# Kernel tuning notes

Hardware: AMD Instinct MI355X
Metric: run time of the kernel (lower is better)

Reference implementation:

```python
import jax, jax.numpy as jnp
import numpy as np

B, T, D, UNITS = 32, 2048, 1024, 1024


def setup_inputs() -> dict:
    key = jax.random.key(0)
    ks = jax.random.split(key, 9)
    values = jax.random.normal(ks[0], (B, T, D), dtype=jnp.float32)
    query = jax.random.normal(ks[1], (B, D), dtype=jnp.float32)
    # mask: 1.0 where position is masked out, 0.0 otherwise
    mask = jax.random.randint(ks[2], (B, T), 0, 2).astype(jnp.float32)
    # Dense params (keras Dense: y = x @ W + b)
    W1 = jax.random.normal(ks[3], (D, UNITS), dtype=jnp.float32) / np.sqrt(D)
    b1 = jnp.zeros((UNITS,), dtype=jnp.float32)
    W2 = jax.random.normal(ks[4], (D, UNITS), dtype=jnp.float32) / np.sqrt(D)
    b2 = jnp.zeros((UNITS,), dtype=jnp.float32)
    V = jax.random.normal(ks[5], (UNITS, 1), dtype=jnp.float32) / np.sqrt(UNITS)
    bV = jnp.zeros((1,), dtype=jnp.float32)
    return {"values": values, "query": query, "mask": mask,
            "W1": W1, "b1": b1, "W2": W2, "b2": b2, "V": V, "bV": bV}


def reference(values, query, mask, W1, b1, W2, b2, V, bV):
    # values: [B,T,D], query: [B,D], mask: [B,T] (1.0 = masked)
    proj_v = jnp.einsum('btd,du->btu', values, W1) + b1          # [B,T,U]
    proj_q = (query @ W2 + b2)[:, None, :]                        # [B,1,U]
    score = jnp.tanh(proj_v + proj_q) @ V + bV                    # [B,T,1]
    score = score + mask[:, :, None] * (-1e9)                     # mask out
    attention_weights = jax.nn.softmax(score, axis=1)             # [B,T,1]
    context_vector = jnp.sum(attention_weights * values, axis=1)  # [B,D]
    return (context_vector, attention_weights)
```

## Files before the change

### kernel.cpp

```cpp
#include <hip/hip_runtime.h>
#include <hip/hip_bf16.h>


typedef __bf16 bf16x8 __attribute__((ext_vector_type(8)));
typedef __bf16 bf16x4 __attribute__((ext_vector_type(4)));
typedef float  f32x4  __attribute__((ext_vector_type(4)));

#define B_  32
#define T_  2048
#define D_  1024
#define U_  1024
#define BT_ (B_*T_)

#define WS_W1T    ((size_t)0)
#define WS_PROJQ  ((size_t)(2u*1024*1024))
#define WS_SCORE  ((size_t)(2u*1024*1024 + 128u*1024))
#define WS_VALB   ((size_t)(4u*1024*1024))
#define WS_NEEDED (WS_VALB + (size_t)BT_ * D_ * 2)

__device__ __forceinline__ float tanh_fast(float x) {
    const float e = __expf(2.0f * x);
    return 1.0f - __fdividef(2.0f, e + 1.0f);
}

__device__ __forceinline__ void glls16(const void* g, void* l) {
    __builtin_amdgcn_global_load_lds(
        (const __attribute__((address_space(1))) void*)g,
        (__attribute__((address_space(3))) void*)l, 16, 0, 0);
}

__global__ void init_kernel(const float* __restrict__ b1, const float* __restrict__ b2,
                            float* __restrict__ projq, float* __restrict__ score) {
    int i = blockIdx.x * 256 + threadIdx.x;
    if (i < B_ * U_) {
        projq[i] = b1[i & (U_ - 1)] + b2[i & (U_ - 1)];
    } else {
        score[i - B_ * U_] = 0.0f;
    }
}

__global__ void convert_kernel(const float* __restrict__ v, __bf16* __restrict__ o) {
    const size_t i = ((size_t)blockIdx.x * 256 + threadIdx.x) * 8;
    const float4 a = *(const float4*)(v + i);
    const float4 b = *(const float4*)(v + i + 4);
    bf16x8 h;
    h[0] = (__bf16)a.x; h[1] = (__bf16)a.y; h[2] = (__bf16)a.z; h[3] = (__bf16)a.w;
    h[4] = (__bf16)b.x; h[5] = (__bf16)b.y; h[6] = (__bf16)b.z; h[7] = (__bf16)b.w;
    *(bf16x8*)(o + i) = h;
}

__global__ void w1_transpose_kernel(const float* __restrict__ W1, __bf16* __restrict__ W1T) {
    __shared__ float tile[64][65];
    const int bx = blockIdx.x & 15;
    const int by = blockIdx.x >> 4;
    const int tid = threadIdx.x;
    const int j  = tid & 63;
    const int i0 = tid >> 6;
#pragma unroll
    for (int p = 0; p < 16; ++p) {
        const int i = i0 + p * 4;
        tile[i][j] = W1[(size_t)(by * 64 + i) * U_ + bx * 64 + j];
    }
    __syncthreads();
#pragma unroll
    for (int p = 0; p < 16; ++p) {
        const int i = i0 + p * 4;
        W1T[(size_t)(bx * 64 + i) * D_ + by * 64 + j] = (__bf16)tile[j][i];
    }
}

__global__ void projq_kernel(const float* __restrict__ query, const float* __restrict__ W2,
                             float* __restrict__ projq) {
    __shared__ float q[128];
    const int b  = blockIdx.x >> 3;
    const int dc = blockIdx.x & 7;
    const int tid = threadIdx.x;
    if (tid < 128) q[tid] = query[(size_t)b * D_ + dc * 128 + tid];
    __syncthreads();
    const int u0 = tid * 4;
    float a0 = 0.f, a1 = 0.f, a2 = 0.f, a3 = 0.f;
    for (int d = 0; d < 128; ++d) {
        const float4 w = *(const float4*)(W2 + (size_t)(dc * 128 + d) * U_ + u0);
        const float qd = q[d];
        a0 = fmaf(qd, w.x, a0); a1 = fmaf(qd, w.y, a1);
        a2 = fmaf(qd, w.z, a2); a3 = fmaf(qd, w.w, a3);
    }
    float* p = projq + (size_t)b * U_ + u0;
    atomicAdd(p + 0, a0); atomicAdd(p + 1, a1);
    atomicAdd(p + 2, a2); atomicAdd(p + 3, a3);
}

__global__ __launch_bounds__(256, 4)
void score_kernel_bf16(const __bf16* __restrict__ valb, const __bf16* __restrict__ W1T,
                       const float* __restrict__ projq, const float* __restrict__ V,
                       float* __restrict__ score) {
    __shared__ __attribute__((aligned(16))) __bf16 Al[128 * 32];
    __shared__ __attribute__((aligned(16))) __bf16 Bl[128 * 32];

    const int tid = threadIdx.x;
    const int xcd  = blockIdx.x & 7;
    const int slot = blockIdx.x >> 3;
    const int rowblk = xcd * 64 + (slot >> 3);
    const int utile  = slot & 7;
    const int wave = tid >> 6, lane = tid & 63;
    const int quad = lane >> 4, l15 = lane & 15;
    const int wr = (wave >> 1) * 64;
    const int wc = (wave & 1) * 64;

    const __bf16* Ab = valb + ((size_t)rowblk * 128 + (tid >> 2)) * D_ + (tid & 3) * 8;
    const __bf16* Bb = W1T + ((size_t)utile * 128 + (tid >> 2)) * D_ + (tid & 3) * 8;
    __bf16* Ald = Al + wave * 512;
    __bf16* Bld = Bl + wave * 512;

    f32x4 acc[4][4];
#pragma unroll
    for (int i = 0; i < 4; ++i)
#pragma unroll
        for (int j = 0; j < 4; ++j) {
            f32x4 z = {0.f, 0.f, 0.f, 0.f};
            acc[i][j] = z;
        }

    for (int kk = 0; kk < D_; kk += 32) {
        glls16(Ab + kk,            Ald);
        glls16(Ab + 64 * D_ + kk,  Ald + 2048);
        glls16(Bb + kk,            Bld);
        glls16(Bb + 64 * D_ + kk,  Bld + 2048);
        __syncthreads();

        bf16x8 af[4];
#pragma unroll
        for (int mt = 0; mt < 4; ++mt)
            af[mt] = *(const bf16x8*)(Al + (wr + mt * 16 + l15) * 32 + quad * 8);
#pragma unroll
        for (int nt = 0; nt < 4; ++nt) {
            const bf16x8 bfr = *(const bf16x8*)(Bl + (wc + nt * 16 + l15) * 32 + quad * 8);
#pragma unroll
            for (int mt = 0; mt < 4; ++mt)
                acc[mt][nt] = __builtin_amdgcn_mfma_f32_16x16x32_bf16(af[mt], bfr, acc[mt][nt], 0, 0, 0);
        }
        __syncthreads();
    }

    const int b = rowblk >> 4;
    const float* pq = projq + (size_t)b * U_ + utile * 128 + wc;
    const float* Vp = V + utile * 128 + wc;
    const size_t rowbase = (size_t)rowblk * 128 + wr;
#pragma unroll
    for (int mt = 0; mt < 4; ++mt) {
        float s0 = 0.f, s1 = 0.f, s2 = 0.f, s3 = 0.f;
#pragma unroll
        for (int nt = 0; nt < 4; ++nt) {
            const int u = nt * 16 + l15;
            const float pqu = pq[u];
            const float vu  = Vp[u];
            s0 += tanh_fast(acc[mt][nt][0] + pqu) * vu;
            s1 += tanh_fast(acc[mt][nt][1] + pqu) * vu;
            s2 += tanh_fast(acc[mt][nt][2] + pqu) * vu;
            s3 += tanh_fast(acc[mt][nt][3] + pqu) * vu;
        }
        float s[4] = {s0, s1, s2, s3};
#pragma unroll
        for (int r = 0; r < 4; ++r) {
            float v = s[r];
            v += __shfl_xor(v, 1);
            v += __shfl_xor(v, 2);
            v += __shfl_xor(v, 4);
            v += __shfl_xor(v, 8);
            if (l15 == 0)
                atomicAdd(&score[rowbase + mt * 16 + quad * 4 + r], v);
        }
    }
}

__global__ __launch_bounds__(512, 2)
void score_kernel_f32(const float* __restrict__ values, const __bf16* __restrict__ W1T,
                      const float* __restrict__ projq, const float* __restrict__ V,
                      float* __restrict__ score) {
    __shared__ __attribute__((aligned(16))) __bf16 Al[64][40];
    __shared__ __attribute__((aligned(16))) __bf16 Bl[512][40];
    const int tid    = threadIdx.x;
    const int rowblk = blockIdx.x >> 1;
    const int nhalf  = blockIdx.x & 1;
    const int wave = tid >> 6, lane = tid & 63;
    const int quad = lane >> 4, l15 = lane & 15;
    const float*  Abase = values + (size_t)rowblk * 64 * D_;
    const __bf16* Bbase = W1T + (size_t)nhalf * 512 * D_;
    const int ar = tid >> 3, ac = (tid & 7) * 4;
    const int br = tid >> 2, bc = (tid & 3) * 8;
    f32x4 acc[4][4];
#pragma unroll
    for (int i = 0; i < 4; ++i)
#pragma unroll
        for (int j = 0; j < 4; ++j) { f32x4 z = {0.f,0.f,0.f,0.f}; acc[i][j] = z; }
    for (int kk = 0; kk < D_; kk += 32) {
        {
            const float4 v = *(const float4*)(Abase + (size_t)ar * D_ + kk + ac);
            bf16x4 h;
            h[0] = (__bf16)v.x; h[1] = (__bf16)v.y; h[2] = (__bf16)v.z; h[3] = (__bf16)v.w;
            *(bf16x4*)(&Al[ar][ac]) = h;
        }
#pragma unroll
        for (int p = 0; p < 4; ++p) {
            const int rr = p * 128 + br;
            const bf16x8 w = *(const bf16x8*)(Bbase + (size_t)rr * D_ + kk + bc);
            *(bf16x8*)(&Bl[rr][bc]) = w;
        }
        __syncthreads();
        bf16x8 af[4];
#pragma unroll
        for (int mt = 0; mt < 4; ++mt)
            af[mt] = *(const bf16x8*)(&Al[mt * 16 + l15][quad * 8]);
#pragma unroll
        for (int nt = 0; nt < 4; ++nt) {
            const bf16x8 bfr = *(const bf16x8*)(&Bl[wave * 64 + nt * 16 + l15][quad * 8]);
#pragma unroll
            for (int mt = 0; mt < 4; ++mt)
                acc[mt][nt] = __builtin_amdgcn_mfma_f32_16x16x32_bf16(af[mt], bfr, acc[mt][nt], 0, 0, 0);
        }
        __syncthreads();
    }
    const int b = rowblk >> 5;
    const size_t rowbase = (size_t)rowblk * 64;
    const float* pq = projq + (size_t)b * U_;
    const int ub = nhalf * 512 + wave * 64;
#pragma unroll
    for (int mt = 0; mt < 4; ++mt) {
        float s0 = 0.f, s1 = 0.f, s2 = 0.f, s3 = 0.f;
#pragma unroll
        for (int nt = 0; nt < 4; ++nt) {
            const int u = ub + nt * 16 + l15;
            const float pqu = pq[u];
            const float vu  = V[u];
            s0 += tanh_fast(acc[mt][nt][0] + pqu) * vu;
            s1 += tanh_fast(acc[mt][nt][1] + pqu) * vu;
            s2 += tanh_fast(acc[mt][nt][2] + pqu) * vu;
            s3 += tanh_fast(acc[mt][nt][3] + pqu) * vu;
        }
        float s[4] = {s0, s1, s2, s3};
#pragma unroll
        for (int r = 0; r < 4; ++r) {
            float v = s[r];
            v += __shfl_xor(v, 1);
            v += __shfl_xor(v, 2);
            v += __shfl_xor(v, 4);
            v += __shfl_xor(v, 8);
            if (l15 == 0)
                atomicAdd(&score[rowbase + mt * 16 + quad * 4 + r], v);
        }
    }
}

__global__ void softmax_kernel(const float* __restrict__ score, const float* __restrict__ mask,
                               const float* __restrict__ bV, float* __restrict__ out) {
    const int b = blockIdx.x;
    const int tid = threadIdx.x;
    const float bv = bV[0];
    float s[8];
    float lmax = -3.0e38f;
#pragma unroll
    for (int i = 0; i < 8; ++i) {
        const int t = tid + i * 256;
        const float v = score[(size_t)b * T_ + t] + bv + mask[(size_t)b * T_ + t] * (-1.0e9f);
        s[i] = v;
        lmax = fmaxf(lmax, v);
    }
#pragma unroll
    for (int m = 1; m < 64; m <<= 1) lmax = fmaxf(lmax, __shfl_xor(lmax, m));
    __shared__ float redm[4], reds[4];
    if ((tid & 63) == 0) redm[tid >> 6] = lmax;
    __syncthreads();
    const float M = fmaxf(fmaxf(redm[0], redm[1]), fmaxf(redm[2], redm[3]));
    float lsum = 0.f;
#pragma unroll
    for (int i = 0; i < 8; ++i) { s[i] = __expf(s[i] - M); lsum += s[i]; }
#pragma unroll
    for (int m = 1; m < 64; m <<= 1) lsum += __shfl_xor(lsum, m);
    if ((tid & 63) == 0) reds[tid >> 6] = lsum;
    __syncthreads();
    const float inv = 1.0f / (reds[0] + reds[1] + reds[2] + reds[3]);
#pragma unroll
    for (int i = 0; i < 8; ++i)
        out[(size_t)B_ * D_ + (size_t)b * T_ + tid + i * 256] = s[i] * inv;
}

__global__ void context_kernel(const float* __restrict__ values, const float* __restrict__ attn,
                               float* __restrict__ out) {
    const int b  = blockIdx.x >> 4;
    const int dc = blockIdx.x & 15;
    const int tid = threadIdx.x;
    __shared__ float a[T_];
#pragma unroll
    for (int i = 0; i < 8; ++i) a[tid + i * 256] = attn[(size_t)b * T_ + tid + i * 256];
    __syncthreads();
    const int dl = (tid & 15) * 4;
    const int tg = tid >> 4;
    const float* vb = values + (size_t)b * T_ * D_ + dc * 64 + dl;
    f32x4 acc = {0.f, 0.f, 0.f, 0.f};
#pragma unroll 4
    for (int t = tg; t < T_; t += 16) {
        const float4 v = *(const float4*)(vb + (size_t)t * D_);
        const float w = a[t];
        acc[0] = fmaf(w, v.x, acc[0]);
        acc[1] = fmaf(w, v.y, acc[1]);
        acc[2] = fmaf(w, v.z, acc[2]);
        acc[3] = fmaf(w, v.w, acc[3]);
    }
    __shared__ __attribute__((aligned(16))) float red[16][64];
    *(f32x4*)(&red[tg][dl]) = acc;
    __syncthreads();
    if (tid < 64) {
        float s = 0.f;
#pragma unroll
        for (int g = 0; g < 16; ++g) s += red[g][tid];
        out[(size_t)b * D_ + dc * 64 + tid] = s;
    }
}

extern "C" void kernel_launch(void* const* d_in, const int* in_sizes, int n_in,
                              void* d_out, int out_size, void* d_ws, size_t ws_size,
                              hipStream_t stream) {
    const float* values = (const float*)d_in[0];
    const float* query  = (const float*)d_in[1];
    const float* mask   = (const float*)d_in[2];
    const float* W1     = (const float*)d_in[3];
    const float* b1     = (const float*)d_in[4];
    const float* W2     = (const float*)d_in[5];
    const float* b2     = (const float*)d_in[6];
    const float* V      = (const float*)d_in[7];
    const float* bV     = (const float*)d_in[8];
    float* out = (float*)d_out;

    char* ws = (char*)d_ws;
    __bf16* W1T   = (__bf16*)(ws + WS_W1T);
    float*  projq = (float*)(ws + WS_PROJQ);
    float*  score = (float*)(ws + WS_SCORE);
    __bf16* valb  = (__bf16*)(ws + WS_VALB);

    init_kernel<<<dim3(384), dim3(256), 0, stream>>>(b1, b2, projq, score);
    w1_transpose_kernel<<<dim3(256), dim3(256), 0, stream>>>(W1, W1T);
    projq_kernel<<<dim3(256), dim3(256), 0, stream>>>(query, W2, projq);
    if (ws_size >= WS_NEEDED) {
        convert_kernel<<<dim3(32768), dim3(256), 0, stream>>>(values, valb);
        score_kernel_bf16<<<dim3(4096), dim3(256), 0, stream>>>(valb, W1T, projq, V, score);
    } else {
        score_kernel_f32<<<dim3(2048), dim3(512), 0, stream>>>(values, W1T, projq, V, score);
    }
    softmax_kernel<<<dim3(32), dim3(256), 0, stream>>>(score, mask, bV, out);
    context_kernel<<<dim3(512), dim3(256), 0, stream>>>(values, out + B_ * D_, out);
}
```

Measured before the change: 637.3 us.

## Replace bf16 score GEMM with 256x256 double-buffered phased MFMA kernel

Rewrites the bf16 score GEMM to use 256x256 tiles per 512-thread block, with BK=64. It adds double-buffered LDS with async global-to-LDS loads issued ahead of compute, an XOR-swizzled LDS layout, and raw ds_read_b128. MFMA work is split into four phases with barriers and setprio so loads overlap the math. This targets LDS/global bandwidth and load latency in the previous 128x128 single-buffered loop. The cost is higher register and LDS pressure, plus fragile hand-tuned waitcnt sequencing.

```diff
diff --git a/kernel.cpp b/kernel.cpp
--- a/kernel.cpp
+++ b/kernel.cpp
@@ -4,6 +4,7 @@
 
 typedef __bf16 bf16x8 __attribute__((ext_vector_type(8)));
 typedef __bf16 bf16x4 __attribute__((ext_vector_type(4)));
+typedef short  s16x8  __attribute__((ext_vector_type(8)));
 typedef float  f32x4  __attribute__((ext_vector_type(4)));
 
 #define B_  32
@@ -90,74 +91,143 @@
     atomicAdd(p + 2, a2); atomicAdd(p + 3, a3);
 }
 
-__global__ __launch_bounds__(256, 4)
-void score_kernel_bf16(const __bf16* __restrict__ valb, const __bf16* __restrict__ W1T,
-                       const float* __restrict__ projq, const float* __restrict__ V,
-                       float* __restrict__ score) {
-    __shared__ __attribute__((aligned(16))) __bf16 Al[128 * 32];
-    __shared__ __attribute__((aligned(16))) __bf16 Bl[128 * 32];
-
-    const int tid = threadIdx.x;
-    const int xcd  = blockIdx.x & 7;
-    const int slot = blockIdx.x >> 3;
-    const int rowblk = xcd * 64 + (slot >> 3);
-    const int utile  = slot & 7;
-    const int wave = tid >> 6, lane = tid & 63;
-    const int quad = lane >> 4, l15 = lane & 15;
-    const int wr = (wave >> 1) * 64;
-    const int wc = (wave & 1) * 64;
-
-    const __bf16* Ab = valb + ((size_t)rowblk * 128 + (tid >> 2)) * D_ + (tid & 3) * 8;
-    const __bf16* Bb = W1T + ((size_t)utile * 128 + (tid >> 2)) * D_ + (tid & 3) * 8;
-    __bf16* Ald = Al + wave * 512;
-    __bf16* Bld = Bl + wave * 512;
-
-    f32x4 acc[4][4];
-#pragma unroll
-    for (int i = 0; i < 4; ++i)
-#pragma unroll
-        for (int j = 0; j < 4; ++j) {
-            f32x4 z = {0.f, 0.f, 0.f, 0.f};
-            acc[i][j] = z;
-        }
-
-    for (int kk = 0; kk < D_; kk += 32) {
-        glls16(Ab + kk,            Ald);
-        glls16(Ab + 64 * D_ + kk,  Ald + 2048);
-        glls16(Bb + kk,            Bld);
-        glls16(Bb + 64 * D_ + kk,  Bld + 2048);
-        __syncthreads();
-
-        bf16x8 af[4];
-#pragma unroll
-        for (int mt = 0; mt < 4; ++mt)
-            af[mt] = *(const bf16x8*)(Al + (wr + mt * 16 + l15) * 32 + quad * 8);
+
+#define SC_LDSB 32768
+
+__global__ __launch_bounds__(512, 2)
+void score_kernel_8ph(const __bf16* __restrict__ valb, const __bf16* __restrict__ W1T,
+                      const float* __restrict__ projq, const float* __restrict__ V,
+                      float* __restrict__ score) {
+    __shared__ __attribute__((aligned(16))) __bf16 lds[2 * SC_LDSB];
+
+    const int tid  = threadIdx.x;
+    const int bid  = blockIdx.x;
+    const int xcd  = bid & 7;
+    const int sl   = bid >> 3;
+    const int mblk = xcd * 32 + (sl >> 2);
+    const int nblk = sl & 3;
+
+    const int wv   = tid >> 6;
+    const int lane = tid & 63;
+    const int wm   = wv >> 2;
+    const int wn   = wv & 3;
+    const int l15  = lane & 15, quad = lane >> 4;
+    const int e    = l15 & 7;
+    const int sl0  = ((quad)     ^ e) * 8;
+    const int sl1  = ((quad + 4) ^ e) * 8;
+    const int offA0 = wm * 8192 + l15 * 64 + sl0;
+    const int offA1 = wm * 8192 + l15 * 64 + sl1;
+    const int offB0 = 16384 + (wn >> 1) * 8192 + ((wn & 1) * 64 + l15) * 64 + sl0;
+    const int offB1 = 16384 + (wn >> 1) * 8192 + ((wn & 1) * 64 + l15) * 64 + sl1;
+
+    const int srow = lane >> 3;
+    const int scol = ((lane & 7) ^ srow) * 8;
+    const __bf16* aS = valb + ((size_t)mblk * 256 + wv * 8 + srow) * D_ + scol;
+    const __bf16* bS = W1T  + ((size_t)nblk * 256 + wv * 8 + srow) * D_ + scol;
+    __bf16* aD = lds + wv * 512;
+    __bf16* bD = lds + 16384 + wv * 512;
+
+#define DSR(dst, off) do { s16x8 _t;                                            \
+    asm volatile("ds_read_b128 %0, %1" : "=v"(_t)                              \
+        : "v"((const __attribute__((address_space(3))) __bf16*)(lds + (off)))); \
+    (dst) = __builtin_bit_cast(bf16x8, _t); } while (0)
+
+#define STA(CB, H, KT) do {                                                     \
+    glls16(aS + (size_t)((H)*128     ) * D_ + (KT)*64, aD + (CB) + (H)*8192);        \
+    glls16(aS + (size_t)((H)*128 + 64) * D_ + (KT)*64, aD + (CB) + (H)*8192 + 4096); \
+    } while (0)
+#define STB(CB, H, KT) do {                                                     \
+    glls16(bS + (size_t)((H)*128     ) * D_ + (KT)*64, bD + (CB) + (H)*8192);        \
+    glls16(bS + (size_t)((H)*128 + 64) * D_ + (KT)*64, bD + (CB) + (H)*8192 + 4096); \
+    } while (0)
+
+#define PH_SYNC do { __builtin_amdgcn_s_barrier();                              \
+    asm volatile("s_waitcnt lgkmcnt(0)" ::: "memory");                          \
+    __builtin_amdgcn_sched_barrier(0);                                          \
+    __builtin_amdgcn_s_setprio(1); } while (0)
+#define PH_END do { __builtin_amdgcn_s_setprio(0);                              \
+    __builtin_amdgcn_s_barrier(); } while (0)
+
+#define MQ(ML, NL) do {                                                         \
+    _Pragma("unroll") for (int mi = 0; mi < 4; ++mi)                            \
+    _Pragma("unroll") for (int ni = 0; ni < 2; ++ni) {                          \
+        acc[(ML)+mi][(NL)+ni] = __builtin_amdgcn_mfma_f32_16x16x32_bf16(        \
+            afr[mi][0], bfr[(NL)+ni][0], acc[(ML)+mi][(NL)+ni], 0, 0, 0);       \
+        acc[(ML)+mi][(NL)+ni] = __builtin_amdgcn_mfma_f32_16x16x32_bf16(        \
+            afr[mi][1], bfr[(NL)+ni][1], acc[(ML)+mi][(NL)+ni], 0, 0, 0);       \
+    } } while (0)
+
+#define TILE(KT, CB, DOA, DOB, VM) do {                                         \
+                                 \
+    _Pragma("unroll") for (int m = 0; m < 4; ++m) {                             \
+        DSR(afr[m][0], (CB) + offA0 + m*1024);                                  \
+        DSR(afr[m][1], (CB) + offA1 + m*1024); }                                \
+    _Pragma("unroll") for (int n = 0; n < 2; ++n) {                             \
+        DSR(bfr[n][0], (CB) + offB0 + n*1024);                                  \
+        DSR(bfr[n][1], (CB) + offB1 + n*1024); }                                \
+    if (DOA) STA((CB) ^ SC_LDSB, 0, (KT)+1);                                    \
+    PH_SYNC; MQ(0, 0); PH_END;                                                  \
+                                          \
+    _Pragma("unroll") for (int n = 0; n < 2; ++n) {                             \
+        DSR(bfr[2+n][0], (CB) + offB0 + (2+n)*1024);                            \
+        DSR(bfr[2+n][1], (CB) + offB1 + (2+n)*1024); }                          \
+    if (DOA) STA((CB) ^ SC_LDSB, 1, (KT)+1);                                    \
+    PH_SYNC; MQ(0, 2); PH_END;                                                  \
+                                          \
+    _Pragma("unroll") for (int m = 0; m < 4; ++m) {                             \
+        DSR(afr[m][0], (CB) + offA0 + (4+m)*1024);                              \
+        DSR(afr[m][1], (CB) + offA1 + (4+m)*1024); }                            \
+    if (DOB) STB((CB), 0, (KT)+2);                                              \
+    PH_SYNC; MQ(4, 0); PH_END;                                                  \
+             \
+    if (DOB) STB((CB), 1, (KT)+2);                                              \
+    __builtin_amdgcn_s_barrier();                                               \
+    __builtin_amdgcn_sched_barrier(0);                                          \
+    __builtin_amdgcn_s_setprio(1);                                              \
+    MQ(4, 2);                                                                   \
+    __builtin_amdgcn_s_setprio(0);                                              \
+    if ((VM) == 4)      asm volatile("s_waitcnt vmcnt(4)" ::: "memory");        \
+    else if ((VM) == 0) asm volatile("s_waitcnt vmcnt(0)" ::: "memory");        \
+    __builtin_amdgcn_s_barrier();                                               \
+} while (0)
+
+    bf16x8 afr[4][2];
+    bf16x8 bfr[4][2];
+    f32x4  acc[8][4];
+#pragma unroll
+    for (int i = 0; i < 8; ++i)
+#pragma unroll
+        for (int j = 0; j < 4; ++j) { f32x4 z = {0.f, 0.f, 0.f, 0.f}; acc[i][j] = z; }
+
+    STA(0, 0, 0); STA(0, 1, 0); STB(0, 0, 0); STB(0, 1, 0);
+    STB(SC_LDSB, 0, 1); STB(SC_LDSB, 1, 1);
+    asm volatile("s_waitcnt vmcnt(4)" ::: "memory");
+    __builtin_amdgcn_s_barrier();
+
+#pragma unroll 1
+    for (int tt = 0; tt < 14; tt += 2) {
+        TILE(tt,     0,       1, 1, 4);
+        TILE(tt + 1, SC_LDSB, 1, 1, 4);
+    }
+    TILE(14, 0,       1, 0, 0);
+    TILE(15, SC_LDSB, 0, 0, -1);
+
+    const int bq = mblk >> 3;
+    const float* pq = projq + (size_t)bq * U_ + nblk * 256 + wn * 64;
+    const float* Vp = V + nblk * 256 + wn * 64;
+    float pqu[4], vu[4];
+#pragma unroll
+    for (int nt = 0; nt < 4; ++nt) { pqu[nt] = pq[nt * 16 + l15]; vu[nt] = Vp[nt * 16 + l15]; }
+    const size_t rowbase = (size_t)mblk * 256 + (size_t)wm * 128;
+#pragma unroll
+    for (int mt = 0; mt < 8; ++mt) {
+        float s0 = 0.f, s1 = 0.f, s2 = 0.f, s3 = 0.f;
 #pragma unroll
         for (int nt = 0; nt < 4; ++nt) {
-            const bf16x8 bfr = *(const bf16x8*)(Bl + (wc + nt * 16 + l15) * 32 + quad * 8);
-#pragma unroll
-            for (int mt = 0; mt < 4; ++mt)
-                acc[mt][nt] = __builtin_amdgcn_mfma_f32_16x16x32_bf16(af[mt], bfr, acc[mt][nt], 0, 0, 0);
-        }
-        __syncthreads();
-    }
-
-    const int b = rowblk >> 4;
-    const float* pq = projq + (size_t)b * U_ + utile * 128 + wc;
-    const float* Vp = V + utile * 128 + wc;
-    const size_t rowbase = (size_t)rowblk * 128 + wr;
-#pragma unroll
-    for (int mt = 0; mt < 4; ++mt) {
-        float s0 = 0.f, s1 = 0.f, s2 = 0.f, s3 = 0.f;
-#pragma unroll
-        for (int nt = 0; nt < 4; ++nt) {
-            const int u = nt * 16 + l15;
-            const float pqu = pq[u];
-            const float vu  = Vp[u];
-            s0 += tanh_fast(acc[mt][nt][0] + pqu) * vu;
-            s1 += tanh_fast(acc[mt][nt][1] + pqu) * vu;
-            s2 += tanh_fast(acc[mt][nt][2] + pqu) * vu;
-            s3 += tanh_fast(acc[mt][nt][3] + pqu) * vu;
+            s0 += tanh_fast(acc[mt][nt][0] + pqu[nt]) * vu[nt];
+            s1 += tanh_fast(acc[mt][nt][1] + pqu[nt]) * vu[nt];
+            s2 += tanh_fast(acc[mt][nt][2] + pqu[nt]) * vu[nt];
+            s3 += tanh_fast(acc[mt][nt][3] + pqu[nt]) * vu[nt];
         }
         float s[4] = {s0, s1, s2, s3};
 #pragma unroll
@@ -171,6 +241,13 @@
                 atomicAdd(&score[rowbase + mt * 16 + quad * 4 + r], v);
         }
     }
+#undef DSR
+#undef STA
+#undef STB
+#undef PH_SYNC
+#undef PH_END
+#undef MQ
+#undef TILE
 }
 
 __global__ __launch_bounds__(512, 2)
@@ -342,7 +419,7 @@
     projq_kernel<<<dim3(256), dim3(256), 0, stream>>>(query, W2, projq);
     if (ws_size >= WS_NEEDED) {
         convert_kernel<<<dim3(32768), dim3(256), 0, stream>>>(values, valb);
-        score_kernel_bf16<<<dim3(4096), dim3(256), 0, stream>>>(valb, W1T, projq, V, score);
+        score_kernel_8ph<<<dim3(1024), dim3(512), 0, stream>>>(valb, W1T, projq, V, score);
     } else {
         score_kernel_f32<<<dim3(2048), dim3(512), 0, stream>>>(values, W1T, projq, V, score);
     }
```

Result: faster. 615.4 us (-3.4%).

## Double-buffer score GEMM with 128x256 tiles, swizzled LDS, and bf16 context read

Applied to the files above, without the earlier changes.

Replaces the bf16 score GEMM with a 512-thread kernel that computes 128x256 output tiles and double-buffers the LDS stages so the next K-slice is loaded while the current one runs on MFMA. A single barrier per step replaces two, and an XOR swizzle on LDS slots is meant to cut bank conflicts. The context reduction now reads the bf16 copy of values instead of fp32, which halves that kernel's memory traffic but adds bf16 rounding error to the context output. The larger LDS footprint and register use may lower occupancy.

```diff
diff --git a/kernel.cpp b/kernel.cpp
--- a/kernel.cpp
+++ b/kernel.cpp
@@ -90,74 +90,96 @@
     atomicAdd(p + 2, a2); atomicAdd(p + 3, a3);
 }
 
-__global__ __launch_bounds__(256, 4)
-void score_kernel_bf16(const __bf16* __restrict__ valb, const __bf16* __restrict__ W1T,
-                       const float* __restrict__ projq, const float* __restrict__ V,
-                       float* __restrict__ score) {
-    __shared__ __attribute__((aligned(16))) __bf16 Al[128 * 32];
-    __shared__ __attribute__((aligned(16))) __bf16 Bl[128 * 32];
-
-    const int tid = threadIdx.x;
-    const int xcd  = blockIdx.x & 7;
-    const int slot = blockIdx.x >> 3;
-    const int rowblk = xcd * 64 + (slot >> 3);
-    const int utile  = slot & 7;
-    const int wave = tid >> 6, lane = tid & 63;
-    const int quad = lane >> 4, l15 = lane & 15;
-    const int wr = (wave >> 1) * 64;
-    const int wc = (wave & 1) * 64;
-
-    const __bf16* Ab = valb + ((size_t)rowblk * 128 + (tid >> 2)) * D_ + (tid & 3) * 8;
-    const __bf16* Bb = W1T + ((size_t)utile * 128 + (tid >> 2)) * D_ + (tid & 3) * 8;
-    __bf16* Ald = Al + wave * 512;
-    __bf16* Bld = Bl + wave * 512;
+
+#define SC_A_ELE 4096
+#define SC_B_ELE 8192
+#define SC_BUF   (SC_A_ELE + SC_B_ELE)
+
+__global__ __launch_bounds__(512, 4)
+void score_kernel_occ(const __bf16* __restrict__ valb, const __bf16* __restrict__ W1T,
+                      const float* __restrict__ projq, const float* __restrict__ V,
+                      float* __restrict__ score) {
+    __shared__ __attribute__((aligned(16))) __bf16 lds[2 * SC_BUF];
+
+    const int tid  = threadIdx.x;
+    const int bid  = blockIdx.x;
+    const int xcd  = bid & 7;
+    const int sl   = bid >> 3;
+    const int mblk = xcd * 64 + (sl >> 2);
+    const int nblk = sl & 3;
+
+    const int wv   = tid >> 6;
+    const int lane = tid & 63;
+    const int wm   = wv >> 2;
+    const int wn   = wv & 3;
+    const int l15  = lane & 15, quad = lane >> 4;
+
+    const int rslot = (quad ^ ((l15 >> 1) & 3)) * 8;
+
+    const int srow = lane >> 2;
+    const int slog = ((lane & 3) ^ ((srow >> 1) & 3)) * 8;
+    const __bf16* aS = valb + ((size_t)mblk * 128 + wv * 16 + srow) * D_ + slog;
+    const __bf16* bS = W1T  + ((size_t)nblk * 256 + wv * 16 + srow) * D_ + slog;
+    __bf16* aD = lds + wv * 512;
+    __bf16* bD = lds + SC_A_ELE + wv * 512;
+
+#define STAGE(CB, KT) do {                                                      \
+    glls16(aS + (KT) * 32,                    aD + (CB));                       \
+    glls16(bS + (KT) * 32,                    bD + (CB));                       \
+    glls16(bS + (size_t)128 * D_ + (KT) * 32, bD + (CB) + 4096);                \
+    } while (0)
+
+#define BODY(KT, CB, DOS) do {                                                  \
+    if (DOS) STAGE((CB) ^ SC_BUF, (KT) + 1);                                    \
+    bf16x8 af[4], bf[4];                                                        \
+    _Pragma("unroll")                                                           \
+    for (int mt = 0; mt < 4; ++mt)                                              \
+        af[mt] = *(const bf16x8*)(lds + (CB) +                                  \
+                   (wm * 64 + mt * 16 + l15) * 32 + rslot);                     \
+    _Pragma("unroll")                                                           \
+    for (int nt = 0; nt < 4; ++nt)                                              \
+        bf[nt] = *(const bf16x8*)(lds + (CB) + SC_A_ELE +                       \
+                   (wn * 64 + nt * 16 + l15) * 32 + rslot);                     \
+    _Pragma("unroll")                                                           \
+    for (int nt = 0; nt < 4; ++nt)                                              \
+    _Pragma("unroll")                                                           \
+    for (int mt = 0; mt < 4; ++mt)                                              \
+        acc[mt][nt] = __builtin_amdgcn_mfma_f32_16x16x32_bf16(                  \
+            af[mt], bf[nt], acc[mt][nt], 0, 0, 0);                              \
+    __syncthreads();                                                            \
+    } while (0)
 
     f32x4 acc[4][4];
 #pragma unroll
     for (int i = 0; i < 4; ++i)
 #pragma unroll
-        for (int j = 0; j < 4; ++j) {
-            f32x4 z = {0.f, 0.f, 0.f, 0.f};
-            acc[i][j] = z;
-        }
-
-    for (int kk = 0; kk < D_; kk += 32) {
-        glls16(Ab + kk,            Ald);
-        glls16(Ab + 64 * D_ + kk,  Ald + 2048);
-        glls16(Bb + kk,            Bld);
-        glls16(Bb + 64 * D_ + kk,  Bld + 2048);
-        __syncthreads();
-
-        bf16x8 af[4];
-#pragma unroll
-        for (int mt = 0; mt < 4; ++mt)
-            af[mt] = *(const bf16x8*)(Al + (wr + mt * 16 + l15) * 32 + quad * 8);
-#pragma unroll
-        for (int nt = 0; nt < 4; ++nt) {
-            const bf16x8 bfr = *(const bf16x8*)(Bl + (wc + nt * 16 + l15) * 32 + quad * 8);
-#pragma unroll
-            for (int mt = 0; mt < 4; ++mt)
-                acc[mt][nt] = __builtin_amdgcn_mfma_f32_16x16x32_bf16(af[mt], bfr, acc[mt][nt], 0, 0, 0);
-        }
-        __syncthreads();
-    }
-
-    const int b = rowblk >> 4;
-    const float* pq = projq + (size_t)b * U_ + utile * 128 + wc;
-    const float* Vp = V + utile * 128 + wc;
-    const size_t rowbase = (size_t)rowblk * 128 + wr;
+        for (int j = 0; j < 4; ++j) { f32x4 z = {0.f, 0.f, 0.f, 0.f}; acc[i][j] = z; }
+
+    STAGE(0, 0);
+    __syncthreads();
+
+#pragma unroll 1
+    for (int kt = 0; kt < 32; kt += 2) {
+        BODY(kt,     0,      1);
+        BODY(kt + 1, SC_BUF, (kt + 1) < 31);
+    }
+
+    const int bq = mblk >> 4;
+    const float* pq = projq + (size_t)bq * U_ + nblk * 256 + wn * 64;
+    const float* Vp = V + nblk * 256 + wn * 64;
+    float pqu[4], vu[4];
+#pragma unroll
+    for (int nt = 0; nt < 4; ++nt) { pqu[nt] = pq[nt * 16 + l15]; vu[nt] = Vp[nt * 16 + l15]; }
+    const size_t rowbase = (size_t)mblk * 128 + (size_t)wm * 64;
 #pragma unroll
     for (int mt = 0; mt < 4; ++mt) {
         float s0 = 0.f, s1 = 0.f, s2 = 0.f, s3 = 0.f;
 #pragma unroll
         for (int nt = 0; nt < 4; ++nt) {
-            const int u = nt * 16 + l15;
-            const float pqu = pq[u];
-            const float vu  = Vp[u];
-            s0 += tanh_fast(acc[mt][nt][0] + pqu) * vu;
-            s1 += tanh_fast(acc[mt][nt][1] + pqu) * vu;
-            s2 += tanh_fast(acc[mt][nt][2] + pqu) * vu;
-            s3 += tanh_fast(acc[mt][nt][3] + pqu) * vu;
+            s0 += tanh_fast(acc[mt][nt][0] + pqu[nt]) * vu[nt];
+            s1 += tanh_fast(acc[mt][nt][1] + pqu[nt]) * vu[nt];
+            s2 += tanh_fast(acc[mt][nt][2] + pqu[nt]) * vu[nt];
+            s3 += tanh_fast(acc[mt][nt][3] + pqu[nt]) * vu[nt];
         }
         float s[4] = {s0, s1, s2, s3};
 #pragma unroll
@@ -171,6 +193,8 @@
                 atomicAdd(&score[rowbase + mt * 16 + quad * 4 + r], v);
         }
     }
+#undef STAGE
+#undef BODY
 }
 
 __global__ __launch_bounds__(512, 2)
@@ -284,6 +308,40 @@
         out[(size_t)B_ * D_ + (size_t)b * T_ + tid + i * 256] = s[i] * inv;
 }
 
+__global__ void context_kernel_bf16(const __bf16* __restrict__ valb, const float* __restrict__ attn,
+                                    float* __restrict__ out) {
+    const int b  = blockIdx.x >> 4;
+    const int dc = blockIdx.x & 15;
+    const int tid = threadIdx.x;
+    __shared__ float a[T_];
+#pragma unroll
+    for (int i = 0; i < 8; ++i) a[tid + i * 256] = attn[(size_t)b * T_ + tid + i * 256];
+    __syncthreads();
+    const int dl = (tid & 7) * 8;
+    const int tg = tid >> 3;
+    const __bf16* vb = valb + (size_t)b * T_ * D_ + dc * 64 + dl;
+    float acc[8];
+#pragma unroll
+    for (int j = 0; j < 8; ++j) acc[j] = 0.f;
+#pragma unroll 4
+    for (int t = tg; t < T_; t += 32) {
+        const bf16x8 v = *(const bf16x8*)(vb + (size_t)t * D_);
+        const float w = a[t];
+#pragma unroll
+        for (int j = 0; j < 8; ++j) acc[j] = fmaf(w, (float)v[j], acc[j]);
+    }
+    __shared__ __attribute__((aligned(16))) float red[32][65];
+#pragma unroll
+    for (int j = 0; j < 8; ++j) red[tg][dl + j] = acc[j];
+    __syncthreads();
+    if (tid < 64) {
+        float s = 0.f;
+#pragma unroll
+        for (int g = 0; g < 32; ++g) s += red[g][tid];
+        out[(size_t)b * D_ + dc * 64 + tid] = s;
+    }
+}
+
 __global__ void context_kernel(const float* __restrict__ values, const float* __restrict__ attn,
                                float* __restrict__ out) {
     const int b  = blockIdx.x >> 4;
@@ -342,10 +400,12 @@
     projq_kernel<<<dim3(256), dim3(256), 0, stream>>>(query, W2, projq);
     if (ws_size >= WS_NEEDED) {
         convert_kernel<<<dim3(32768), dim3(256), 0, stream>>>(values, valb);
-        score_kernel_bf16<<<dim3(4096), dim3(256), 0, stream>>>(valb, W1T, projq, V, score);
+        score_kernel_occ<<<dim3(2048), dim3(512), 0, stream>>>(valb, W1T, projq, V, score);
+        softmax_kernel<<<dim3(32), dim3(256), 0, stream>>>(score, mask, bV, out);
+        context_kernel_bf16<<<dim3(512), dim3(256), 0, stream>>>(valb, out + B_ * D_, out);
     } else {
         score_kernel_f32<<<dim3(2048), dim3(512), 0, stream>>>(values, W1T, projq, V, score);
-    }
-    softmax_kernel<<<dim3(32), dim3(256), 0, stream>>>(score, mask, bV, out);
-    context_kernel<<<dim3(512), dim3(256), 0, stream>>>(values, out + B_ * D_, out);
-}
+        softmax_kernel<<<dim3(32), dim3(256), 0, stream>>>(score, mask, bV, out);
+        context_kernel<<<dim3(512), dim3(256), 0, stream>>>(values, out + B_ * D_, out);
+    }
+}
```

Result: faster. 606.3 us (-4.9%).
